# Optimization experiments

Hardware: AMD Instinct MI355X
Metric: run time of the kernel (lower is better)

## Reference

```python
import jax, jax.numpy as jnp
import numpy as np

H = 64  # hidden_size
IN = 9  # input_size == output_size
PRED_LEN = 10
SRC_LEN = 7
B = 65536


def _lstm_step(x, h, c, Wih, Whh, b):
    # PyTorch gate order: i, f, g, o
    gates = x @ Wih.T + h @ Whh.T + b  # (B, 4H)
    i, f, g, o = jnp.split(gates, 4, axis=-1)
    i = jax.nn.sigmoid(i)
    f = jax.nn.sigmoid(f)
    g = jnp.tanh(g)
    o = jax.nn.sigmoid(o)
    c_new = f * c + i * g
    h_new = o * jnp.tanh(c_new)
    return h_new, c_new


def setup_inputs() -> dict:
    key = jax.random.key(0)
    ks = jax.random.split(key, 9)
    s = 1.0 / np.sqrt(H)  # torch LSTM init scale
    return {
        "src": jax.random.normal(ks[0], (B, SRC_LEN, IN), dtype=jnp.float32),
        "enc_Wih": jax.random.normal(ks[1], (4 * H, IN), dtype=jnp.float32) * s,
        "enc_Whh": jax.random.normal(ks[2], (4 * H, H), dtype=jnp.float32) * s,
        "enc_b": jax.random.normal(ks[3], (4 * H,), dtype=jnp.float32) * s,
        "dec_Wih": jax.random.normal(ks[4], (4 * H, IN), dtype=jnp.float32) * s,
        "dec_Whh": jax.random.normal(ks[5], (4 * H, H), dtype=jnp.float32) * s,
        "dec_b": jax.random.normal(ks[6], (4 * H,), dtype=jnp.float32) * s,
        "fc_W": jax.random.normal(ks[7], (IN, H), dtype=jnp.float32) * s,
        "fc_b": jax.random.normal(ks[8], (IN,), dtype=jnp.float32) * s,
    }


def reference(src, enc_Wih, enc_Whh, enc_b, dec_Wih, dec_Whh, dec_b, fc_W, fc_b):
    b = src.shape[0]
    h0 = jnp.zeros((b, H), dtype=src.dtype)
    c0 = jnp.zeros((b, H), dtype=src.dtype)

    # Encoder: scan over the 7 source timesteps
    def enc_f(carry, x_t):
        h, c = carry
        h, c = _lstm_step(x_t, h, c, enc_Wih, enc_Whh, enc_b)
        return (h, c), None

    (h, c), _ = jax.lax.scan(enc_f, (h0, c0), jnp.swapaxes(src, 0, 1))

    x_last = src[:, -1, :]  # (B, IN)

    def dec_f(carry, _):
        h, c, x = carry
        h, c = _lstm_step(x, h, c, dec_Wih, dec_Whh, dec_b)
        pred = h @ fc_W.T + fc_b  # (B, IN)
        return (h, c, pred), pred

    _, preds = jax.lax.scan(dec_f, (h, c, x_last), None, length=PRED_LEN)
    return jnp.swapaxes(preds, 0, 1)  # (B, PRED_LEN, IN)
```

## Files before the change

### kernel.cpp

```cpp
#include <hip/hip_runtime.h>
#include <hip/hip_bf16.h>
#include <stdint.h>

namespace {
constexpr int kH = 64;
constexpr int kIn = 9;
constexpr int kSrcLen = 7;
constexpr int kPredLen = 10;
constexpr int kRows = 64;
constexpr int kThreads = 256;
constexpr int kOutW = kPredLen * kIn;
constexpr int kBiasK = 73;
constexpr int kABlk = 12;
constexpr int kASz = kABlk * kRows * 8;

typedef __attribute__((ext_vector_type(8))) _Float16 frag_a;
typedef __attribute__((ext_vector_type(4))) float frag_cd;

__device__ __forceinline__ float fast_rcp(float x) { return __builtin_amdgcn_rcpf(x); }
__device__ __forceinline__ float sigmoid_f(float x) { return fast_rcp(1.0f + __expf(-x)); }
__device__ __forceinline__ float tanh_f(float x) { return 1.0f - 2.0f * fast_rcp(__expf(2.0f * x) + 1.0f); }

__device__ __forceinline__ float ldf(const void* p, int i, int isbf) {
  if (isbf) {
    uint32_t w = ((uint32_t)((const uint16_t*)p)[i]) << 16;
    float f; __builtin_memcpy(&f, &w, 4); return f;
  }
  return ((const float*)p)[i];
}

__device__ __forceinline__ float gate_w(const void* Whh, const void* Wih,
                                        const void* bv, int n, int k, int isbf) {
  if (k < kH) return ldf(Whh, n * kH + k, isbf);
  if (k < kH + kIn) return ldf(Wih, n * kIn + (k - kH), isbf);
  if (k == kBiasK) return ldf(bv, n, isbf);
  return 0.0f;
}
}

extern "C" __global__ void detect_dtype_kernel(const uint16_t* __restrict__ src_u16,
                                               int* __restrict__ flag) {
  const int t = threadIdx.x;
  int bad = 0;
  for (int i = t; i < 256; i += 64) {
    const uint16_t u = src_u16[i];
    const uint32_t e = (u >> 7) & 0xFF;
    const int plausible = (u == 0) || (e >= 100 && e <= 150);
    bad += !plausible;
  }
#pragma unroll
  for (int off = 32; off; off >>= 1) bad += __shfl_down(bad, off, 64);
  if (t == 0) *flag = (bad < 64) ? 1 : 0;
}

extern "C" __global__ void __launch_bounds__(kThreads)
__attribute__((amdgpu_waves_per_eu(3, 3)))
lstm_seq2seq_kernel(const void* __restrict__ src,
                    const void* __restrict__ enc_Wih,
                    const void* __restrict__ enc_Whh,
                    const void* __restrict__ enc_b,
                    const void* __restrict__ dec_Wih,
                    const void* __restrict__ dec_Whh,
                    const void* __restrict__ dec_b,
                    const void* __restrict__ fc_W,
                    const void* __restrict__ fc_b,
                    void* __restrict__ out,
                    const int* __restrict__ flag) {
  __shared__ __align__(16) _Float16 a_m[2][kASz];

  const int tid = threadIdx.x;
  const int lane = tid & 63;
  const int wave = tid >> 6;
  const int quad = lane >> 4;
  const int half = lane & 15;
  const int row0 = blockIdx.x * kRows;
  const int isbf = *flag;
  const int col = wave * 16 + half;

  for (int i = tid; i < kASz; i += kThreads) {
    const int e = i & 7;
    const int blk = i / (kRows * 8);
    const _Float16 v = (blk == 9 && e == 1) ? (_Float16)1.0f : (_Float16)0.0f;
    a_m[0][i] = v;
    a_m[1][i] = v;
  }
  __syncthreads();

  const int it1_on = (tid + 256 < kRows * kIn);
  const int it2_on = (tid + 512 < kRows * kIn);
  const int r_0 = tid / kIn, i_0 = tid - r_0 * kIn;
  const int r_1 = (tid + 256) / kIn, i_1 = (tid + 256) - r_1 * kIn;
  const int r_2 = (tid + 512) / kIn, i_2 = (tid + 512) - r_2 * kIn;
  const int lds0 = (((8 + (i_0 >> 3)) * kRows) + r_0) * 8 + (i_0 & 7);
  const int lds1 = (((8 + (i_1 >> 3)) * kRows) + r_1) * 8 + (i_1 & 7);
  const int lds2 = (((8 + (i_2 >> 3)) * kRows) + r_2) * 8 + (i_2 & 7);
  const int g0 = (row0 + r_0) * (kSrcLen * kIn) + i_0;
  const int g1 = (row0 + r_1) * (kSrcLen * kIn) + i_1;
  const int g2 = (row0 + r_2) * (kSrcLen * kIn) + i_2;

  {
    a_m[0][lds0] = (_Float16)ldf(src, g0, isbf);
    if (it1_on) a_m[0][lds1] = (_Float16)ldf(src, g1, isbf);
    if (it2_on) a_m[0][lds2] = (_Float16)ldf(src, g2, isbf);
  }

  float c_st[16];
#pragma unroll
  for (int i = 0; i < 16; ++i) c_st[i] = 0.0f;

  frag_a bm[3][4];
  frag_a fm[2];
  float fcb = 0.0f;

  auto load_gate_frags = [&](const void* Whh, const void* Wih, const void* bv) {
#pragma unroll
    for (int kt = 0; kt < 3; ++kt) {
#pragma unroll
      for (int nt = 0; nt < 4; ++nt) {
        frag_a f;
        const int n = nt * kH + col;
#pragma unroll
        for (int j = 0; j < 8; ++j) {
          const int k = kt * 32 + quad * 8 + j;
          f[j] = (_Float16)gate_w(Whh, Wih, bv, n, k, isbf);
        }
        bm[kt][nt] = f;
      }
    }
  };

  auto lstm_step = [&](int cur) {
#pragma unroll 1
    for (int ch = 0; ch < 4; ++ch) {
      const int r = ch * 16 + half;
      const frag_a a0 = *(const frag_a*)&a_m[cur][((0 * 4 + quad) * kRows + r) * 8];
      const frag_a a1 = *(const frag_a*)&a_m[cur][((1 * 4 + quad) * kRows + r) * 8];
      const frag_a a2 = *(const frag_a*)&a_m[cur][((2 * 4 + quad) * kRows + r) * 8];

      frag_cd acc[4];
#pragma unroll
      for (int nt = 0; nt < 4; ++nt) {
        frag_cd a = {0.f, 0.f, 0.f, 0.f};
        a = __builtin_amdgcn_mfma_f32_16x16x32_f16(a0, bm[0][nt], a, 0, 0, 0);
        a = __builtin_amdgcn_mfma_f32_16x16x32_f16(a1, bm[1][nt], a, 0, 0, 0);
        a = __builtin_amdgcn_mfma_f32_16x16x32_f16(a2, bm[2][nt], a, 0, 0, 0);
        acc[nt] = a;
      }

#pragma unroll
      for (int j = 0; j < 4; ++j) {
        const float gi = acc[0][j];
        const float gf = acc[1][j];
        const float gg = acc[2][j];
        const float go = acc[3][j];
        float c = c_st[ch * 4 + j];
        c = fmaf(sigmoid_f(gf), c, sigmoid_f(gi) * tanh_f(gg));
        c_st[ch * 4 + j] = c;
        const float h = sigmoid_f(go) * tanh_f(c);
        const int rr = ch * 16 + quad * 4 + j;
        a_m[cur ^ 1][(((col >> 3) * kRows) + rr) * 8 + (col & 7)] = (_Float16)h;
      }
    }
  };

  load_gate_frags(enc_Whh, enc_Wih, enc_b);
  __syncthreads();

  int cur = 0;
#pragma unroll 1
  for (int s = 0; s < kSrcLen; ++s) {
    const int ns = (s + 1 < kSrcLen) ? s + 1 : kSrcLen - 1;
    const int off = ns * kIn;
    const float x0 = ldf(src, g0 + off, isbf);
    const float x1 = it1_on ? ldf(src, g1 + off, isbf) : 0.0f;
    const float x2 = it2_on ? ldf(src, g2 + off, isbf) : 0.0f;

    lstm_step(cur);

    a_m[cur ^ 1][lds0] = (_Float16)x0;
    if (it1_on) a_m[cur ^ 1][lds1] = (_Float16)x1;
    if (it2_on) a_m[cur ^ 1][lds2] = (_Float16)x2;
    __syncthreads();
    cur ^= 1;
  }

  load_gate_frags(dec_Whh, dec_Wih, dec_b);
#pragma unroll
  for (int kt = 0; kt < 2; ++kt) {
    frag_a f;
#pragma unroll
    for (int j = 0; j < 8; ++j) {
      const int k = kt * 32 + quad * 8 + j;
      const float v = (half < kIn) ? ldf(fc_W, half * kH + k, isbf) : 0.0f;
      f[j] = (_Float16)v;
    }
    fm[kt] = f;
  }
  fcb = (half < kIn) ? ldf(fc_b, half, isbf) : 0.0f;

#pragma unroll 1
  for (int t = 0; t < kPredLen; ++t) {
    lstm_step(cur);
    __syncthreads();
    cur ^= 1;

    const int r = wave * 16 + half;
    const frag_a a0 = *(const frag_a*)&a_m[cur][((0 * 4 + quad) * kRows + r) * 8];
    const frag_a a1 = *(const frag_a*)&a_m[cur][((1 * 4 + quad) * kRows + r) * 8];
    frag_cd p = {fcb, fcb, fcb, fcb};
    p = __builtin_amdgcn_mfma_f32_16x16x32_f16(a0, fm[0], p, 0, 0, 0);
    p = __builtin_amdgcn_mfma_f32_16x16x32_f16(a1, fm[1], p, 0, 0, 0);

    if (half < kIn) {
#pragma unroll
      for (int j = 0; j < 4; ++j) {
        const int rr = wave * 16 + quad * 4 + j;
        const float pred = p[j];
        const int oidx = (row0 + rr) * kOutW + t * kIn + half;
        if (isbf) {
          ((__hip_bfloat16*)out)[oidx] = __float2bfloat16(pred);
        } else {
          ((float*)out)[oidx] = pred;
        }
        a_m[cur][(((8 + (half >> 3)) * kRows) + rr) * 8 + (half & 7)] = (_Float16)pred;
      }
    }
    __syncthreads();
  }
}

extern "C" void kernel_launch(void* const* d_in, const int* in_sizes, int n_in,
                              void* d_out, int out_size, void* d_ws, size_t ws_size,
                              hipStream_t stream) {
  (void)n_in; (void)ws_size; (void)out_size;
  int* flag = (int*)d_ws;

  hipLaunchKernelGGL(detect_dtype_kernel, dim3(1), dim3(64), 0, stream,
                     (const uint16_t*)d_in[0], flag);

  const int b_total = in_sizes[0] / (kSrcLen * kIn);
  const int grid = b_total / kRows;

  hipLaunchKernelGGL(lstm_seq2seq_kernel, dim3(grid), dim3(kThreads), 0, stream,
                     d_in[0], d_in[1], d_in[2], d_in[3], d_in[4], d_in[5],
                     d_in[6], d_in[7], d_in[8], d_out, flag);
}
```

Measured before the change: 250.2 us.

## Shrink input/bias K-tile to 16x16x16 MFMA and raise occupancy to four waves

The x and bias columns move out of the 32-wide third K tile into a separate 16-wide LDS buffer, and that part of the gate GEMM now uses mfma_f32_16x16x16f16 instead of a 16x16x32 MFMA. This drops padded zero work and shrinks the register-held weight fragments, which lets waves_per_eu go from 3 to 4. The bias is now folded in as column 9 of the x buffer. The risk is register spilling at the tighter occupancy target, and the extra LDS buffer changes how accesses map to banks.

```diff
diff --git a/kernel.cpp b/kernel.cpp
--- a/kernel.cpp
+++ b/kernel.cpp
@@ -10,11 +10,12 @@
 constexpr int kRows = 64;
 constexpr int kThreads = 256;
 constexpr int kOutW = kPredLen * kIn;
-constexpr int kBiasK = 73;
-constexpr int kABlk = 12;
+constexpr int kABlk = 8;
 constexpr int kASz = kABlk * kRows * 8;
+constexpr int kAxSz = kRows * 16;
 
 typedef __attribute__((ext_vector_type(8))) _Float16 frag_a;
+typedef __attribute__((ext_vector_type(4))) _Float16 frag_a2;
 typedef __attribute__((ext_vector_type(4))) float frag_cd;
 
 __device__ __forceinline__ float fast_rcp(float x) { return __builtin_amdgcn_rcpf(x); }
@@ -27,14 +28,6 @@
     float f; __builtin_memcpy(&f, &w, 4); return f;
   }
   return ((const float*)p)[i];
-}
-
-__device__ __forceinline__ float gate_w(const void* Whh, const void* Wih,
-                                        const void* bv, int n, int k, int isbf) {
-  if (k < kH) return ldf(Whh, n * kH + k, isbf);
-  if (k < kH + kIn) return ldf(Wih, n * kIn + (k - kH), isbf);
-  if (k == kBiasK) return ldf(bv, n, isbf);
-  return 0.0f;
 }
 }
 
@@ -54,7 +47,7 @@
 }
 
 extern "C" __global__ void __launch_bounds__(kThreads)
-__attribute__((amdgpu_waves_per_eu(3, 3)))
+__attribute__((amdgpu_waves_per_eu(4, 4)))
 lstm_seq2seq_kernel(const void* __restrict__ src,
                     const void* __restrict__ enc_Wih,
                     const void* __restrict__ enc_Whh,
@@ -67,6 +60,7 @@
                     void* __restrict__ out,
                     const int* __restrict__ flag) {
   __shared__ __align__(16) _Float16 a_m[2][kASz];
+  __shared__ __align__(16) _Float16 ax[2][kAxSz];
 
   const int tid = threadIdx.x;
   const int lane = tid & 63;
@@ -78,11 +72,13 @@
   const int col = wave * 16 + half;
 
   for (int i = tid; i < kASz; i += kThreads) {
-    const int e = i & 7;
-    const int blk = i / (kRows * 8);
-    const _Float16 v = (blk == 9 && e == 1) ? (_Float16)1.0f : (_Float16)0.0f;
-    a_m[0][i] = v;
-    a_m[1][i] = v;
+    a_m[0][i] = (_Float16)0.0f;
+    a_m[1][i] = (_Float16)0.0f;
+  }
+  for (int i = tid; i < kAxSz; i += kThreads) {
+    const _Float16 v = ((i & 15) == 9) ? (_Float16)1.0f : (_Float16)0.0f;
+    ax[0][i] = v;
+    ax[1][i] = v;
   }
   __syncthreads();
 
@@ -91,41 +87,48 @@
   const int r_0 = tid / kIn, i_0 = tid - r_0 * kIn;
   const int r_1 = (tid + 256) / kIn, i_1 = (tid + 256) - r_1 * kIn;
   const int r_2 = (tid + 512) / kIn, i_2 = (tid + 512) - r_2 * kIn;
-  const int lds0 = (((8 + (i_0 >> 3)) * kRows) + r_0) * 8 + (i_0 & 7);
-  const int lds1 = (((8 + (i_1 >> 3)) * kRows) + r_1) * 8 + (i_1 & 7);
-  const int lds2 = (((8 + (i_2 >> 3)) * kRows) + r_2) * 8 + (i_2 & 7);
+  const int lds0 = r_0 * 16 + i_0;
+  const int lds1 = r_1 * 16 + i_1;
+  const int lds2 = r_2 * 16 + i_2;
   const int g0 = (row0 + r_0) * (kSrcLen * kIn) + i_0;
   const int g1 = (row0 + r_1) * (kSrcLen * kIn) + i_1;
   const int g2 = (row0 + r_2) * (kSrcLen * kIn) + i_2;
 
-  {
-    a_m[0][lds0] = (_Float16)ldf(src, g0, isbf);
-    if (it1_on) a_m[0][lds1] = (_Float16)ldf(src, g1, isbf);
-    if (it2_on) a_m[0][lds2] = (_Float16)ldf(src, g2, isbf);
-  }
+  ax[0][lds0] = (_Float16)ldf(src, g0, isbf);
+  if (it1_on) ax[0][lds1] = (_Float16)ldf(src, g1, isbf);
+  if (it2_on) ax[0][lds2] = (_Float16)ldf(src, g2, isbf);
 
   float c_st[16];
 #pragma unroll
   for (int i = 0; i < 16; ++i) c_st[i] = 0.0f;
 
-  frag_a bm[3][4];
+  frag_a bm0[4], bm1[4];
+  frag_a2 bm2[4];
   frag_a fm[2];
   float fcb = 0.0f;
 
   auto load_gate_frags = [&](const void* Whh, const void* Wih, const void* bv) {
 #pragma unroll
-    for (int kt = 0; kt < 3; ++kt) {
-#pragma unroll
-      for (int nt = 0; nt < 4; ++nt) {
-        frag_a f;
-        const int n = nt * kH + col;
-#pragma unroll
-        for (int j = 0; j < 8; ++j) {
-          const int k = kt * 32 + quad * 8 + j;
-          f[j] = (_Float16)gate_w(Whh, Wih, bv, n, k, isbf);
-        }
-        bm[kt][nt] = f;
-      }
+    for (int nt = 0; nt < 4; ++nt) {
+      const int n = nt * kH + col;
+      frag_a f0, f1;
+#pragma unroll
+      for (int j = 0; j < 8; ++j) {
+        f0[j] = (_Float16)ldf(Whh, n * kH + (quad * 8 + j), isbf);
+        f1[j] = (_Float16)ldf(Whh, n * kH + (32 + quad * 8 + j), isbf);
+      }
+      bm0[nt] = f0;
+      bm1[nt] = f1;
+      frag_a2 f2;
+#pragma unroll
+      for (int j = 0; j < 4; ++j) {
+        const int k2 = quad * 4 + j;
+        float v = 0.0f;
+        if (k2 < kIn) v = ldf(Wih, n * kIn + k2, isbf);
+        else if (k2 == kIn) v = ldf(bv, n, isbf);
+        f2[j] = (_Float16)v;
+      }
+      bm2[nt] = f2;
     }
   };
 
@@ -135,15 +138,15 @@
       const int r = ch * 16 + half;
       const frag_a a0 = *(const frag_a*)&a_m[cur][((0 * 4 + quad) * kRows + r) * 8];
       const frag_a a1 = *(const frag_a*)&a_m[cur][((1 * 4 + quad) * kRows + r) * 8];
-      const frag_a a2 = *(const frag_a*)&a_m[cur][((2 * 4 + quad) * kRows + r) * 8];
+      const frag_a2 a2 = *(const frag_a2*)&ax[cur][r * 16 + quad * 4];
 
       frag_cd acc[4];
 #pragma unroll
       for (int nt = 0; nt < 4; ++nt) {
         frag_cd a = {0.f, 0.f, 0.f, 0.f};
-        a = __builtin_amdgcn_mfma_f32_16x16x32_f16(a0, bm[0][nt], a, 0, 0, 0);
-        a = __builtin_amdgcn_mfma_f32_16x16x32_f16(a1, bm[1][nt], a, 0, 0, 0);
-        a = __builtin_amdgcn_mfma_f32_16x16x32_f16(a2, bm[2][nt], a, 0, 0, 0);
+        a = __builtin_amdgcn_mfma_f32_16x16x32_f16(a0, bm0[nt], a, 0, 0, 0);
+        a = __builtin_amdgcn_mfma_f32_16x16x32_f16(a1, bm1[nt], a, 0, 0, 0);
+        a = __builtin_amdgcn_mfma_f32_16x16x16f16(a2, bm2[nt], a, 0, 0, 0);
         acc[nt] = a;
       }
 
@@ -177,9 +180,9 @@
 
     lstm_step(cur);
 
-    a_m[cur ^ 1][lds0] = (_Float16)x0;
-    if (it1_on) a_m[cur ^ 1][lds1] = (_Float16)x1;
-    if (it2_on) a_m[cur ^ 1][lds2] = (_Float16)x2;
+    ax[cur ^ 1][lds0] = (_Float16)x0;
+    if (it1_on) ax[cur ^ 1][lds1] = (_Float16)x1;
+    if (it2_on) ax[cur ^ 1][lds2] = (_Float16)x2;
     __syncthreads();
     cur ^= 1;
   }
@@ -191,8 +194,7 @@
 #pragma unroll
     for (int j = 0; j < 8; ++j) {
       const int k = kt * 32 + quad * 8 + j;
-      const float v = (half < kIn) ? ldf(fc_W, half * kH + k, isbf) : 0.0f;
-      f[j] = (_Float16)v;
+      f[j] = (half < kIn) ? (_Float16)ldf(fc_W, half * kH + k, isbf) : (_Float16)0.0f;
     }
     fm[kt] = f;
   }
@@ -222,7 +224,7 @@
         } else {
           ((float*)out)[oidx] = pred;
         }
-        a_m[cur][(((8 + (half >> 3)) * kRows) + rr) * 8 + (half & 7)] = (_Float16)pred;
+        ax[cur][rr * 16 + half] = (_Float16)pred;
       }
     }
     __syncthreads();
```

Measured after the change: 221.4 us. -11.5%, faster.
